# Kernel optimization log

Measured on AMD Instinct MI355X. Metric: run time of the kernel, lower is better.

Reference implementation:

```python
import jax, jax.numpy as jnp
import numpy as np

B, N, D_IN, H, L, HEADS = 8, 1024, 64, 128, 2, 4
HEAD_DIM = H // HEADS
EPS = 1e-5


def setup_inputs() -> dict:
    key = jax.random.key(0)
    ks = jax.random.split(key, 20)
    x = jax.random.normal(ks[0], (B, N, D_IN), dtype=jnp.float32)
    adj = jax.random.randint(ks[1], (B, N, N), 0, 2).astype(jnp.float32)
    s = lambda fan_in: 1.0 / np.sqrt(fan_in)
    enc_w = jax.random.uniform(ks[2], (H, D_IN), minval=-s(D_IN), maxval=s(D_IN))
    enc_b = jax.random.uniform(ks[3], (H,), minval=-s(D_IN), maxval=s(D_IN))
    # per-layer stacked projection weights, torch Linear layout [out,in]
    def mk(k, shape):
        return jax.random.uniform(k, shape, minval=-s(H), maxval=s(H))
    q_w = mk(ks[4], (L, H, H)); q_b = mk(ks[5], (L, H))
    k_w = mk(ks[6], (L, H, H)); k_b = mk(ks[7], (L, H))
    v_w = mk(ks[8], (L, H, H)); v_b = mk(ks[9], (L, H))
    o_w = mk(ks[10], (L, H, H)); o_b = mk(ks[11], (L, H))
    ln_g = jnp.ones((L, H), jnp.float32)
    ln_b = jnp.zeros((L, H), jnp.float32)
    out_w = mk(ks[12], (H, H)); out_b = mk(ks[13], (H,))
    return {"x": x, "adj": adj, "enc_w": enc_w, "enc_b": enc_b,
            "q_w": q_w, "q_b": q_b, "k_w": k_w, "k_b": k_b,
            "v_w": v_w, "v_b": v_b, "o_w": o_w, "o_b": o_b,
            "ln_g": ln_g, "ln_b": ln_b, "out_w": out_w, "out_b": out_b}


def _layernorm(x, g, b):
    mu = jnp.mean(x, axis=-1, keepdims=True)
    var = jnp.var(x, axis=-1, keepdims=True)
    return (x - mu) * jax.lax.rsqrt(var + EPS) * g + b


def _gat_layer(h, adj, qw, qb, kw, kb, vw, vb, ow, ob):
    b, n, _ = h.shape
    q = (h @ qw.T + qb).reshape(b, n, HEADS, HEAD_DIM)
    k = (h @ kw.T + kb).reshape(b, n, HEADS, HEAD_DIM)
    v = (h @ vw.T + vb).reshape(b, n, HEADS, HEAD_DIM)
    scale = HEAD_DIM ** -0.5
    attn = jnp.einsum('bihd,bjhd->bhij', q, k) * scale
    mask = adj[:, None, :, :]  # (b,1,n,n)
    attn = jnp.where(mask == 0, -jnp.inf, attn)
    a = jax.nn.softmax(attn, axis=-1)
    a = jnp.nan_to_num(a, nan=0.0)  # rows with no neighbours -> 0
    out = jnp.einsum('bhij,bjhd->bihd', a, v).reshape(b, n, H)
    return out @ ow.T + ob


def reference(x, adj, enc_w, enc_b, q_w, q_b, k_w, k_b, v_w, v_b,
              o_w, o_b, ln_g, ln_b, out_w, out_b):
    h = jax.nn.relu(x @ enc_w.T + enc_b)
    for i in range(L):
        h_new = _gat_layer(h, adj, q_w[i], q_b[i], k_w[i], k_b[i],
                           v_w[i], v_b[i], o_w[i], o_b[i])
        h = jax.nn.relu(_layernorm(h_new, ln_g[i], ln_b[i])) + h
    return h @ out_w.T + out_b
```

## Files before the change

kernel.cpp:

```cpp
#include <hip/hip_runtime.h>

#define B 8
#define N 1024
#define D_IN 64
#define H 128
#define HEADS 4
#define HD 32
#define L 2
#define EPS 1e-5f
#define NEG_BIG -1e30f
#define SCALE 0.17677669529663687f

typedef __attribute__((ext_vector_type(8))) short bf16x8;
typedef __attribute__((ext_vector_type(4))) float f32x4;

__device__ __forceinline__ unsigned short f2bf(float f) {
    unsigned u = __float_as_uint(f);
    u = u + 0x7fffu + ((u >> 16) & 1u);
    return (unsigned short)(u >> 16);
}
__device__ __forceinline__ float bf2f(unsigned short s) {
    return __uint_as_float(((unsigned)s) << 16);
}
__device__ __forceinline__ void gload_lds16(const void* g, void* l) {
    __builtin_amdgcn_global_load_lds(
        (const __attribute__((address_space(1))) unsigned int*)g,
        (__attribute__((address_space(3))) unsigned int*)l,
        16, 0, 0);
}

__global__ __launch_bounds__(256) void pack_kernel(
    const float* __restrict__ adj, unsigned* __restrict__ mb) {
    int wd = blockIdx.x * 256 + threadIdx.x;
    const float4* src = (const float4*)(adj + (size_t)wd * 32);
    unsigned m = 0;
    #pragma unroll
    for (int c = 0; c < 8; ++c) {
        float4 f = src[c];
        if (f.x != 0.0f) m |= 1u << (c * 4 + 0);
        if (f.y != 0.0f) m |= 1u << (c * 4 + 1);
        if (f.z != 0.0f) m |= 1u << (c * 4 + 2);
        if (f.w != 0.0f) m |= 1u << (c * 4 + 3);
    }
    mb[wd] = m;
}

__global__ __launch_bounds__(256) void prep_kernel(
    const float* __restrict__ x, const float* __restrict__ enc_w,
    const float* __restrict__ q_w, const float* __restrict__ k_w,
    const float* __restrict__ v_w, const float* __restrict__ q_b,
    const float* __restrict__ k_b, const float* __restrict__ v_b,
    const float* __restrict__ o_w, const float* __restrict__ out_w,
    unsigned short* __restrict__ x_bf, unsigned short* __restrict__ wenc,
    unsigned short* __restrict__ wqkv, float* __restrict__ bqkv,
    unsigned short* __restrict__ woh, unsigned short* __restrict__ wol,
    unsigned short* __restrict__ wfh, unsigned short* __restrict__ wfl) {
    int id = blockIdx.x * 256 + threadIdx.x;
    const int XN = B * N * D_IN;
    const int WE = H * D_IN;
    const int WQ = L * 3 * H * H;
    const int BQ = L * 3 * H;
    const int WO = L * H * H;
    const int WF = H * H;
    if (id < XN) { x_bf[id] = f2bf(x[id]); return; }
    id -= XN;
    if (id < WE) { wenc[id] = f2bf(enc_w[id]); return; }
    id -= WE;
    if (id < WQ) {
        int layer = id / (3 * H * H);
        int r = id % (3 * H * H);
        int mat = r / (H * H);
        int e = r % (H * H);
        const float* src = mat == 0 ? q_w : (mat == 1 ? k_w : v_w);
        float f = src[layer * H * H + e];
        if (mat == 0) f *= SCALE;
        wqkv[id] = f2bf(f);
        return;
    }
    id -= WQ;
    if (id < BQ) {
        int layer = id / (3 * H);
        int r = id % (3 * H);
        int mat = r / H;
        int e = r % H;
        const float* src = mat == 0 ? q_b : (mat == 1 ? k_b : v_b);
        float f = src[layer * H + e];
        if (mat == 0) f *= SCALE;
        bqkv[id] = f;
        return;
    }
    id -= BQ;
    if (id < WO) {
        float f = o_w[id];
        unsigned short hi = f2bf(f);
        woh[id] = hi;
        wol[id] = f2bf(f - bf2f(hi));
        return;
    }
    id -= WO;
    if (id < WF) {
        float f = out_w[id];
        unsigned short hi = f2bf(f);
        wfh[id] = hi;
        wfl[id] = f2bf(f - bf2f(hi));
    }
}

__global__ __launch_bounds__(256) void enc_kernel(
    const unsigned short* __restrict__ x_bf, const unsigned short* __restrict__ wenc,
    const float* __restrict__ eb, float* __restrict__ h, unsigned short* __restrict__ h_bf) {
    __shared__ unsigned short wt[H * D_IN];
    __shared__ unsigned short at[64 * D_IN];
    const int t = threadIdx.x;
    const int r0 = blockIdx.x * 64;
    const int w = t >> 6, lane = t & 63, g = lane >> 4, c16 = lane & 15;

    #pragma unroll
    for (int i = 0; i < 4; ++i) {
        int ci = i * 256 + t, row = ci >> 3, cr = ci & 7;
        gload_lds16(wenc + row * 64 + (cr ^ (row & 7)) * 8, (char*)wt + (i * 4 + w) * 1024);
    }
    #pragma unroll
    for (int i = 0; i < 2; ++i) {
        int ci = i * 256 + t, row = ci >> 3, cr = ci & 7;
        gload_lds16(x_bf + (size_t)(r0 + row) * 64 + (cr ^ (row & 7)) * 8,
                    (char*)at + (i * 4 + w) * 1024);
    }
    __syncthreads();

    const int arow = w * 16 + c16;
    bf16x8 a0 = *(const bf16x8*)(at + arow * 64 + ((g ^ (arow & 7)) * 8));
    bf16x8 a1 = *(const bf16x8*)(at + arow * 64 + (((4 + g) ^ (arow & 7)) * 8));
    f32x4 acc[8];
    #pragma unroll
    for (int sub = 0; sub < 8; ++sub) {
        int bcol = sub * 16 + c16;
        bf16x8 b0 = *(const bf16x8*)(wt + bcol * 64 + ((g ^ (bcol & 7)) * 8));
        bf16x8 b1 = *(const bf16x8*)(wt + bcol * 64 + (((4 + g) ^ (bcol & 7)) * 8));
        f32x4 z = {0.f, 0.f, 0.f, 0.f};
        z = __builtin_amdgcn_mfma_f32_16x16x32_bf16(a0, b0, z, 0, 0, 0);
        acc[sub] = __builtin_amdgcn_mfma_f32_16x16x32_bf16(a1, b1, z, 0, 0, 0);
    }
    #pragma unroll
    for (int sub = 0; sub < 8; ++sub) {
        int col = sub * 16 + c16;
        float bias = eb[col];
        #pragma unroll
        for (int rr = 0; rr < 4; ++rr) {
            int row = r0 + w * 16 + g * 4 + rr;
            float v = fmaxf(acc[sub][rr] + bias, 0.0f);
            h[(size_t)row * H + col] = v;
            h_bf[(size_t)row * H + col] = f2bf(v);
        }
    }
}

__global__ __launch_bounds__(256) void qkv_kernel(
    const unsigned short* __restrict__ h_bf, const unsigned short* __restrict__ wqkv_l,
    const float* __restrict__ bqkv_l,
    unsigned short* __restrict__ q, unsigned short* __restrict__ k,
    unsigned short* __restrict__ vT) {
    __shared__ unsigned short wt[192 * 128];
    __shared__ unsigned short at[64 * 128];
    const int t = threadIdx.x;
    const int r0 = (blockIdx.x >> 1) * 64;
    const int ch = blockIdx.x & 1;
    const int w = t >> 6, lane = t & 63, g = lane >> 4, c16 = lane & 15;
    const unsigned short* wsrc = wqkv_l + (size_t)ch * 192 * 128;

    #pragma unroll
    for (int i = 0; i < 12; ++i) {
        int ci = i * 256 + t, row = ci >> 4, cr = ci & 15;
        gload_lds16(wsrc + (size_t)row * 128 + (cr ^ (row & 7)) * 8,
                    (char*)wt + (i * 4 + w) * 1024);
    }
    #pragma unroll
    for (int i = 0; i < 4; ++i) {
        int ci = i * 256 + t, row = ci >> 4, cr = ci & 15;
        gload_lds16(h_bf + (size_t)(r0 + row) * 128 + (cr ^ (row & 7)) * 8,
                    (char*)at + (i * 4 + w) * 1024);
    }
    __syncthreads();

    const int arow = w * 16 + c16;
    bf16x8 a[4];
    #pragma unroll
    for (int ks = 0; ks < 4; ++ks)
        a[ks] = *(const bf16x8*)(at + arow * 128 + (((ks * 4 + g) ^ (arow & 7)) * 8));

    f32x4 acc[12];
    #pragma unroll
    for (int sub = 0; sub < 12; ++sub) {
        int bcol = sub * 16 + c16;
        f32x4 z = {0.f, 0.f, 0.f, 0.f};
        #pragma unroll
        for (int ks = 0; ks < 4; ++ks) {
            bf16x8 bb = *(const bf16x8*)(wt + (size_t)bcol * 128 + (((ks * 4 + g) ^ (bcol & 7)) * 8));
            z = __builtin_amdgcn_mfma_f32_16x16x32_bf16(a[ks], bb, z, 0, 0, 0);
        }
        acc[sub] = z;
    }
    #pragma unroll
    for (int sub = 0; sub < 12; ++sub) {
        int gcol = ch * 192 + sub * 16 + c16;
        int mat = gcol >> 7;
        int colin = gcol & 127;
        float bias = bqkv_l[mat * H + colin];
        if (mat < 2) {
            unsigned short* dst = mat == 0 ? q : k;
            #pragma unroll
            for (int rr = 0; rr < 4; ++rr) {
                int row = r0 + w * 16 + g * 4 + rr;
                dst[(size_t)row * H + colin] = f2bf(acc[sub][rr] + bias);
            }
        } else {
            int hd = colin >> 5, d = colin & 31;
            int bb = r0 >> 10;
            int jbase = (r0 & (N - 1)) + w * 16 + g * 4;
            int pos = (jbase & ~63) + ((((jbase >> 3) & 7) ^ (d & 7)) << 3) + (jbase & 7);
            float v0 = acc[sub][0] + bias, v1 = acc[sub][1] + bias;
            float v2 = acc[sub][2] + bias, v3 = acc[sub][3] + bias;
            unsigned lo, hi;
            asm("v_cvt_pk_bf16_f32 %0, %1, %2" : "=v"(lo) : "v"(v0), "v"(v1));
            asm("v_cvt_pk_bf16_f32 %0, %1, %2" : "=v"(hi) : "v"(v2), "v"(v3));
            uint2 pk2; pk2.x = lo; pk2.y = hi;
            *(uint2*)(vT + ((size_t)(bb * HEADS + hd) * HD + d) * N + pos) = pk2;
        }
    }
}

__global__ __launch_bounds__(256) void attn_kernel(
    const unsigned short* __restrict__ qg, const unsigned short* __restrict__ kg,
    const unsigned short* __restrict__ vTg, const unsigned* __restrict__ mb,
    float* __restrict__ ao) {
    __shared__ unsigned short qt[64 * 32];
    __shared__ unsigned short kt[2][128 * 32];
    __shared__ unsigned short vt[2][32 * 128];
    __shared__ unsigned short pl[4][16 * 136];

    const int bid = blockIdx.x;
    const int itile = bid & 15;
    const int head = (bid >> 4) & 3;
    const int b = bid >> 6;
    const int i0 = itile * 64;
    const int bh = b * HEADS + head;

    const int t = threadIdx.x;
    const int w = t >> 6;
    const int lane = t & 63;
    const int g = lane >> 4;
    const int c16 = lane & 15;

    const int srow = t >> 2;
    const int sch = (t & 3) ^ ((t >> 2) & 3);

    gload_lds16(qg + ((size_t)(b * N + i0 + srow)) * H + head * HD + sch * 8,
                (char*)qt + w * 1024);
    #pragma unroll
    for (int i = 0; i < 2; ++i)
        gload_lds16(kg + ((size_t)(b * N + i * 64 + srow)) * H + head * HD + sch * 8,
                    (char*)kt[0] + i * 4096 + w * 1024);
    #pragma unroll
    for (int i = 0; i < 2; ++i) {
        int d = i * 16 + (t >> 4), c = t & 15;
        gload_lds16(vTg + ((size_t)bh * HD + d) * N + c * 8,
                    (char*)vt[0] + i * 4096 + w * 1024);
    }
    const unsigned* mrow = mb + (size_t)(b * N + i0 + w * 16 + c16) * (N / 32);
    uint4 am = *(const uint4*)mrow;

    __syncthreads();

    const int swq = c16 & 3;
    const bf16x8 qfrag = *(const bf16x8*)(qt + (w * 16 + c16) * 32 + ((g ^ swq) * 8));

    f32x4 oacc[2];
    oacc[0] = (f32x4){0.f, 0.f, 0.f, 0.f};
    oacc[1] = (f32x4){0.f, 0.f, 0.f, 0.f};
    float mrun = NEG_BIG, lrun = 0.0f;

    for (int jt = 0; jt < 8; ++jt) {
        const int cur = jt & 1;
        uint4 amn;
        if (jt < 7) {
            const int j0n = (jt + 1) * 128;
            #pragma unroll
            for (int i = 0; i < 2; ++i)
                gload_lds16(kg + ((size_t)(b * N + j0n + i * 64 + srow)) * H + head * HD + sch * 8,
                            (char*)kt[cur ^ 1] + i * 4096 + w * 1024);
            #pragma unroll
            for (int i = 0; i < 2; ++i) {
                int d = i * 16 + (t >> 4), c = t & 15;
                gload_lds16(vTg + ((size_t)bh * HD + d) * N + j0n + c * 8,
                            (char*)vt[cur ^ 1] + i * 4096 + w * 1024);
            }
            amn = *(const uint4*)(mrow + (jt + 1) * 4);
        }
        f32x4 sacc[8];
        #pragma unroll
        for (int jsub = 0; jsub < 8; ++jsub) {
            bf16x8 kfrag = *(const bf16x8*)(kt[cur] + (jsub * 16 + c16) * 32 + ((g ^ swq) * 8));
            f32x4 z = {0.f, 0.f, 0.f, 0.f};
            sacc[jsub] = __builtin_amdgcn_mfma_f32_16x16x32_bf16(kfrag, qfrag, z, 0, 0, 0);
        }
        float mx = NEG_BIG;
        #pragma unroll
        for (int jsub = 0; jsub < 8; ++jsub) {
            int wsel = jsub >> 1;
            unsigned mw = wsel == 0 ? am.x : wsel == 1 ? am.y : wsel == 2 ? am.z : am.w;
            #pragma unroll
            for (int r = 0; r < 4; ++r) {
                bool alive = (mw >> ((jsub & 1) * 16 + g * 4 + r)) & 1u;
                float s = alive ? sacc[jsub][r] : NEG_BIG;
                sacc[jsub][r] = s;
                mx = fmaxf(mx, s);
            }
        }
        mx = fmaxf(mx, __shfl_xor(mx, 16));
        mx = fmaxf(mx, __shfl_xor(mx, 32));
        float mnew = fmaxf(mrun, mx);
        float sf = __expf(mrun - mnew);
        mrun = mnew;
        float rs = 0.0f;
        #pragma unroll
        for (int jsub = 0; jsub < 8; ++jsub)
            #pragma unroll
            for (int r = 0; r < 4; ++r) {
                float pv = (sacc[jsub][r] > -0.9e30f) ? __expf(sacc[jsub][r] - mnew) : 0.0f;
                sacc[jsub][r] = pv;
                rs += pv;
            }
        rs += __shfl_xor(rs, 16);
        rs += __shfl_xor(rs, 32);
        lrun = lrun * sf + rs;
        #pragma unroll
        for (int jsub = 0; jsub < 8; ++jsub) {
            unsigned lo, hi;
            asm("v_cvt_pk_bf16_f32 %0, %1, %2" : "=v"(lo) : "v"(sacc[jsub][0]), "v"(sacc[jsub][1]));
            asm("v_cvt_pk_bf16_f32 %0, %1, %2" : "=v"(hi) : "v"(sacc[jsub][2]), "v"(sacc[jsub][3]));
            uint2 pk2; pk2.x = lo; pk2.y = hi;
            *(uint2*)(&pl[w][c16 * 136 + jsub * 16 + g * 4]) = pk2;
        }
        #pragma unroll
        for (int dsub = 0; dsub < 2; ++dsub)
            #pragma unroll
            for (int r = 0; r < 4; ++r)
                oacc[dsub][r] *= sf;
        asm volatile("s_waitcnt lgkmcnt(0)" ::: "memory");
        #pragma unroll
        for (int ks = 0; ks < 4; ++ks) {
            bf16x8 pa = *(const bf16x8*)(&pl[w][c16 * 136 + ks * 32 + g * 8]);
            #pragma unroll
            for (int dsub = 0; dsub < 2; ++dsub) {
                int cj = ks * 4 + g;
                bf16x8 va = *(const bf16x8*)(vt[cur] + (dsub * 16 + c16) * 128 +
                                             (cj >> 3) * 64 + (((cj & 7) ^ (c16 & 7)) * 8));
                oacc[dsub] = __builtin_amdgcn_mfma_f32_16x16x32_bf16(va, pa, oacc[dsub], 0, 0, 0);
            }
        }
        if (jt < 7) {
            am = amn;
            __syncthreads();
        }
    }
    float inv = (lrun > 0.0f) ? (1.0f / lrun) : 0.0f;
    #pragma unroll
    for (int dsub = 0; dsub < 2; ++dsub) {
        float4 o;
        o.x = oacc[dsub][0] * inv; o.y = oacc[dsub][1] * inv;
        o.z = oacc[dsub][2] * inv; o.w = oacc[dsub][3] * inv;
        *(float4*)(ao + ((size_t)(b * N + i0 + w * 16 + c16)) * H +
                   head * HD + dsub * 16 + g * 4) = o;
    }
}

__device__ __forceinline__ void stage_split(
    const float* __restrict__ src, unsigned short* hi, unsigned short* lo, int t) {
    #pragma unroll
    for (int it = 0; it < 8; ++it) {
        int idx4 = it * 256 + t;
        int row = idx4 >> 5, c4 = (idx4 & 31) * 4;
        float4 f = ((const float4*)src)[idx4];
        unsigned short h0 = f2bf(f.x), h1 = f2bf(f.y), h2 = f2bf(f.z), h3 = f2bf(f.w);
        unsigned short l0 = f2bf(f.x - bf2f(h0)), l1 = f2bf(f.y - bf2f(h1));
        unsigned short l2 = f2bf(f.z - bf2f(h2)), l3 = f2bf(f.w - bf2f(h3));
        *(unsigned*)(hi + row * 130 + c4)     = (unsigned)h0 | ((unsigned)h1 << 16);
        *(unsigned*)(hi + row * 130 + c4 + 2) = (unsigned)h2 | ((unsigned)h3 << 16);
        *(unsigned*)(lo + row * 130 + c4)     = (unsigned)l0 | ((unsigned)l1 << 16);
        *(unsigned*)(lo + row * 130 + c4 + 2) = (unsigned)l2 | ((unsigned)l3 << 16);
    }
}

__device__ __forceinline__ void split_gemm(
    const unsigned short* ah, const unsigned short* al,
    const unsigned short* wh, const unsigned short* wl,
    int arow, int g, int c16, f32x4* acc) {
    bf16x8 ahf[4], alf[4];
    #pragma unroll
    for (int ks = 0; ks < 4; ++ks) {
        ahf[ks] = *(const bf16x8*)(ah + arow * 130 + ks * 32 + g * 8);
        alf[ks] = *(const bf16x8*)(al + arow * 130 + ks * 32 + g * 8);
    }
    #pragma unroll
    for (int sub = 0; sub < 8; ++sub) {
        int bcol = sub * 16 + c16;
        f32x4 z = {0.f, 0.f, 0.f, 0.f};
        #pragma unroll
        for (int ks = 0; ks < 4; ++ks) {
            bf16x8 bh = *(const bf16x8*)(wh + bcol * 128 + (((ks * 4 + g) ^ (bcol & 7)) * 8));
            bf16x8 bl = *(const bf16x8*)(wl + bcol * 128 + (((ks * 4 + g) ^ (bcol & 7)) * 8));
            z = __builtin_amdgcn_mfma_f32_16x16x32_bf16(ahf[ks], bh, z, 0, 0, 0);
            z = __builtin_amdgcn_mfma_f32_16x16x32_bf16(alf[ks], bh, z, 0, 0, 0);
            z = __builtin_amdgcn_mfma_f32_16x16x32_bf16(ahf[ks], bl, z, 0, 0, 0);
        }
        acc[sub] = z;
    }
}

__device__ __forceinline__ void stage_w(const unsigned short* __restrict__ src,
                                        unsigned short* dst, int t, int w) {
    #pragma unroll
    for (int i = 0; i < 8; ++i) {
        int ci = i * 256 + t, row = ci >> 4, cr = ci & 15;
        gload_lds16(src + (size_t)row * 128 + (cr ^ (row & 7)) * 8,
                    (char*)dst + (i * 4 + w) * 1024);
    }
}

__global__ __launch_bounds__(256) void oln_kernel(
    const float* __restrict__ ao, const unsigned short* __restrict__ woh_l,
    const unsigned short* __restrict__ wol_l, const float* __restrict__ ob,
    const float* __restrict__ lng, const float* __restrict__ lnb,
    float* __restrict__ h, unsigned short* __restrict__ h_bf) {
    __shared__ unsigned short ah[64 * 130], al[64 * 130];
    __shared__ unsigned short wh[128 * 128], wl[128 * 128];
    const int t = threadIdx.x;
    const int r0 = blockIdx.x * 64;
    const int w = t >> 6, lane = t & 63, g = lane >> 4, c16 = lane & 15;

    stage_w(woh_l, wh, t, w);
    stage_w(wol_l, wl, t, w);
    stage_split(ao + (size_t)r0 * H, ah, al, t);
    __syncthreads();

    const int arow = w * 16 + c16;
    f32x4 acc[8];
    split_gemm(ah, al, wh, wl, arow, g, c16, acc);

    float val[8][4], s1[4] = {0, 0, 0, 0}, s2[4] = {0, 0, 0, 0};
    #pragma unroll
    for (int sub = 0; sub < 8; ++sub) {
        int col = sub * 16 + c16;
        float bias = ob[col];
        #pragma unroll
        for (int rr = 0; rr < 4; ++rr) {
            float vv = acc[sub][rr] + bias;
            val[sub][rr] = vv;
            s1[rr] += vv;
            s2[rr] += vv * vv;
        }
    }
    #pragma unroll
    for (int rr = 0; rr < 4; ++rr) {
        #pragma unroll
        for (int off = 1; off < 16; off <<= 1) {
            s1[rr] += __shfl_xor(s1[rr], off);
            s2[rr] += __shfl_xor(s2[rr], off);
        }
    }
    #pragma unroll
    for (int rr = 0; rr < 4; ++rr) {
        float mu = s1[rr] * (1.0f / H);
        float var = s2[rr] * (1.0f / H) - mu * mu;
        float rsn = rsqrtf(var + EPS);
        int row = r0 + w * 16 + g * 4 + rr;
        #pragma unroll
        for (int sub = 0; sub < 8; ++sub) {
            int col = sub * 16 + c16;
            float y = (val[sub][rr] - mu) * rsn * lng[col] + lnb[col];
            float hn = fmaxf(y, 0.0f) + h[(size_t)row * H + col];
            h[(size_t)row * H + col] = hn;
            h_bf[(size_t)row * H + col] = f2bf(hn);
        }
    }
}

__global__ __launch_bounds__(256) void olnfinal_kernel(
    const float* __restrict__ ao, const unsigned short* __restrict__ woh_l,
    const unsigned short* __restrict__ wol_l, const float* __restrict__ ob,
    const float* __restrict__ lng, const float* __restrict__ lnb,
    const float* __restrict__ h, const unsigned short* __restrict__ wfh,
    const unsigned short* __restrict__ wfl, const float* __restrict__ fb,
    float* __restrict__ out) {
    __shared__ unsigned short ah[64 * 130], al[64 * 130];
    __shared__ unsigned short wh[128 * 128], wl[128 * 128];
    const int t = threadIdx.x;
    const int r0 = blockIdx.x * 64;
    const int w = t >> 6, lane = t & 63, g = lane >> 4, c16 = lane & 15;

    stage_w(woh_l, wh, t, w);
    stage_w(wol_l, wl, t, w);
    stage_split(ao + (size_t)r0 * H, ah, al, t);
    __syncthreads();

    const int arow = w * 16 + c16;
    f32x4 acc[8];
    split_gemm(ah, al, wh, wl, arow, g, c16, acc);

    float val[8][4], s1[4] = {0, 0, 0, 0}, s2[4] = {0, 0, 0, 0};
    #pragma unroll
    for (int sub = 0; sub < 8; ++sub) {
        int col = sub * 16 + c16;
        float bias = ob[col];
        #pragma unroll
        for (int rr = 0; rr < 4; ++rr) {
            float vv = acc[sub][rr] + bias;
            val[sub][rr] = vv;
            s1[rr] += vv;
            s2[rr] += vv * vv;
        }
    }
    #pragma unroll
    for (int rr = 0; rr < 4; ++rr) {
        #pragma unroll
        for (int off = 1; off < 16; off <<= 1) {
            s1[rr] += __shfl_xor(s1[rr], off);
            s2[rr] += __shfl_xor(s2[rr], off);
        }
    }
    __syncthreads();
    #pragma unroll
    for (int rr = 0; rr < 4; ++rr) {
        float mu = s1[rr] * (1.0f / H);
        float var = s2[rr] * (1.0f / H) - mu * mu;
        float rsn = rsqrtf(var + EPS);
        int row = w * 16 + g * 4 + rr;
        #pragma unroll
        for (int sub = 0; sub < 8; ++sub) {
            int col = sub * 16 + c16;
            float y = (val[sub][rr] - mu) * rsn * lng[col] + lnb[col];
            float hn = fmaxf(y, 0.0f) + h[(size_t)(r0 + row) * H + col];
            unsigned short hi = f2bf(hn);
            ah[row * 130 + col] = hi;
            al[row * 130 + col] = f2bf(hn - bf2f(hi));
        }
    }
    stage_w(wfh, wh, t, w);
    stage_w(wfl, wl, t, w);
    __syncthreads();

    f32x4 fac[8];
    split_gemm(ah, al, wh, wl, arow, g, c16, fac);
    #pragma unroll
    for (int sub = 0; sub < 8; ++sub) {
        int col = sub * 16 + c16;
        float bias = fb[col];
        #pragma unroll
        for (int rr = 0; rr < 4; ++rr) {
            int row = r0 + w * 16 + g * 4 + rr;
            out[(size_t)row * H + col] = fac[sub][rr] + bias;
        }
    }
}

extern "C" void kernel_launch(void* const* d_in, const int* in_sizes, int n_in,
                              void* d_out, int out_size, void* d_ws, size_t ws_size,
                              hipStream_t stream) {
    const float* x     = (const float*)d_in[0];
    const float* adj   = (const float*)d_in[1];
    const float* enc_w = (const float*)d_in[2];
    const float* enc_b = (const float*)d_in[3];
    const float* q_w   = (const float*)d_in[4];
    const float* q_b   = (const float*)d_in[5];
    const float* k_w   = (const float*)d_in[6];
    const float* k_b   = (const float*)d_in[7];
    const float* v_w   = (const float*)d_in[8];
    const float* v_b   = (const float*)d_in[9];
    const float* o_w   = (const float*)d_in[10];
    const float* o_b   = (const float*)d_in[11];
    const float* ln_g  = (const float*)d_in[12];
    const float* ln_b  = (const float*)d_in[13];
    const float* out_w = (const float*)d_in[14];
    const float* out_b = (const float*)d_in[15];

    const size_t BNH = (size_t)B * N * H;
    float* h  = (float*)d_ws;
    float* ao = h + BNH;
    unsigned short* h_bf = (unsigned short*)(ao + BNH);
    unsigned short* qb = h_bf + BNH;
    unsigned short* kb = qb + BNH;
    unsigned short* vT = kb + BNH;
    unsigned* mbits = (unsigned*)(vT + BNH);
    unsigned short* x_bf = (unsigned short*)(mbits + (size_t)B * N * N / 32);
    unsigned short* wenc = x_bf + (size_t)B * N * D_IN;
    unsigned short* wqkv = wenc + H * D_IN;
    float* bqkv = (float*)(wqkv + (size_t)L * 3 * H * H);
    unsigned short* woh = (unsigned short*)(bqkv + L * 3 * H);
    unsigned short* wol = woh + (size_t)L * H * H;
    unsigned short* wfh = wol + (size_t)L * H * H;
    unsigned short* wfl = wfh + (size_t)H * H;

    pack_kernel<<<B * N * N / 32 / 256, 256, 0, stream>>>(adj, mbits);
    const int prep_total = B * N * D_IN + H * D_IN + L * 3 * H * H + L * 3 * H
                         + L * H * H + H * H;
    prep_kernel<<<(prep_total + 255) / 256, 256, 0, stream>>>(
        x, enc_w, q_w, k_w, v_w, q_b, k_b, v_b, o_w, out_w,
        x_bf, wenc, wqkv, bqkv, woh, wol, wfh, wfl);
    enc_kernel<<<B * N / 64, 256, 0, stream>>>(x_bf, wenc, enc_b, h, h_bf);

    qkv_kernel<<<B * N / 32, 256, 0, stream>>>(h_bf, wqkv, bqkv, qb, kb, vT);
    attn_kernel<<<B * HEADS * (N / 64), 256, 0, stream>>>(qb, kb, vT, mbits, ao);
    oln_kernel<<<B * N / 64, 256, 0, stream>>>(
        ao, woh, wol, o_b, ln_g, ln_b, h, h_bf);
    qkv_kernel<<<B * N / 32, 256, 0, stream>>>(
        h_bf, wqkv + (size_t)3 * H * H, bqkv + 3 * H, qb, kb, vT);
    attn_kernel<<<B * HEADS * (N / 64), 256, 0, stream>>>(qb, kb, vT, mbits, ao);
    olnfinal_kernel<<<B * N / 64, 256, 0, stream>>>(
        ao, woh + (size_t)H * H, wol + (size_t)H * H, o_b + H,
        ln_g + H, ln_b + H, h, wfh, wfl, out_b, (float*)d_out);
}
```

Before: 95.21 us.

## Halve row tiles in enc/oln kernels, use exp2 softmax, add MFMA priority hints

```diff
diff --git a/kernel.cpp b/kernel.cpp
--- a/kernel.cpp
+++ b/kernel.cpp
@@ -9,7 +9,7 @@
 #define L 2
 #define EPS 1e-5f
 #define NEG_BIG -1e30f
-#define SCALE 0.17677669529663687f
+#define QSCALE (0.17677669529663687f * 1.4426950408889634f)
 
 typedef __attribute__((ext_vector_type(8))) short bf16x8;
 typedef __attribute__((ext_vector_type(4))) float f32x4;
@@ -73,7 +73,7 @@
         int e = r % (H * H);
         const float* src = mat == 0 ? q_w : (mat == 1 ? k_w : v_w);
         float f = src[layer * H * H + e];
-        if (mat == 0) f *= SCALE;
+        if (mat == 0) f *= QSCALE;
         wqkv[id] = f2bf(f);
         return;
     }
@@ -85,7 +85,7 @@
         int e = r % H;
         const float* src = mat == 0 ? q_b : (mat == 1 ? k_b : v_b);
         float f = src[layer * H + e];
-        if (mat == 0) f *= SCALE;
+        if (mat == 0) f *= QSCALE;
         bqkv[id] = f;
         return;
     }
@@ -110,31 +110,31 @@
     const unsigned short* __restrict__ x_bf, const unsigned short* __restrict__ wenc,
     const float* __restrict__ eb, float* __restrict__ h, unsigned short* __restrict__ h_bf) {
     __shared__ unsigned short wt[H * D_IN];
-    __shared__ unsigned short at[64 * D_IN];
+    __shared__ unsigned short at[32 * D_IN];
     const int t = threadIdx.x;
-    const int r0 = blockIdx.x * 64;
+    const int r0 = blockIdx.x * 32;
     const int w = t >> 6, lane = t & 63, g = lane >> 4, c16 = lane & 15;
+    const int rw = w & 1, chw = w >> 1;
 
     #pragma unroll
     for (int i = 0; i < 4; ++i) {
         int ci = i * 256 + t, row = ci >> 3, cr = ci & 7;
         gload_lds16(wenc + row * 64 + (cr ^ (row & 7)) * 8, (char*)wt + (i * 4 + w) * 1024);
     }
-    #pragma unroll
-    for (int i = 0; i < 2; ++i) {
-        int ci = i * 256 + t, row = ci >> 3, cr = ci & 7;
+    {
+        int row = t >> 3, cr = t & 7;
         gload_lds16(x_bf + (size_t)(r0 + row) * 64 + (cr ^ (row & 7)) * 8,
-                    (char*)at + (i * 4 + w) * 1024);
-    }
-    __syncthreads();
-
-    const int arow = w * 16 + c16;
+                    (char*)at + w * 1024);
+    }
+    __syncthreads();
+
+    const int arow = rw * 16 + c16;
     bf16x8 a0 = *(const bf16x8*)(at + arow * 64 + ((g ^ (arow & 7)) * 8));
     bf16x8 a1 = *(const bf16x8*)(at + arow * 64 + (((4 + g) ^ (arow & 7)) * 8));
-    f32x4 acc[8];
-    #pragma unroll
-    for (int sub = 0; sub < 8; ++sub) {
-        int bcol = sub * 16 + c16;
+    f32x4 acc[4];
+    #pragma unroll
+    for (int sub = 0; sub < 4; ++sub) {
+        int bcol = chw * 64 + sub * 16 + c16;
         bf16x8 b0 = *(const bf16x8*)(wt + bcol * 64 + ((g ^ (bcol & 7)) * 8));
         bf16x8 b1 = *(const bf16x8*)(wt + bcol * 64 + (((4 + g) ^ (bcol & 7)) * 8));
         f32x4 z = {0.f, 0.f, 0.f, 0.f};
@@ -142,12 +142,12 @@
         acc[sub] = __builtin_amdgcn_mfma_f32_16x16x32_bf16(a1, b1, z, 0, 0, 0);
     }
     #pragma unroll
-    for (int sub = 0; sub < 8; ++sub) {
-        int col = sub * 16 + c16;
+    for (int sub = 0; sub < 4; ++sub) {
+        int col = chw * 64 + sub * 16 + c16;
         float bias = eb[col];
         #pragma unroll
         for (int rr = 0; rr < 4; ++rr) {
-            int row = r0 + w * 16 + g * 4 + rr;
+            int row = r0 + rw * 16 + g * 4 + rr;
             float v = fmaxf(acc[sub][rr] + bias, 0.0f);
             h[(size_t)row * H + col] = v;
             h_bf[(size_t)row * H + col] = f2bf(v);
@@ -297,12 +297,14 @@
             amn = *(const uint4*)(mrow + (jt + 1) * 4);
         }
         f32x4 sacc[8];
+        __builtin_amdgcn_s_setprio(1);
         #pragma unroll
         for (int jsub = 0; jsub < 8; ++jsub) {
             bf16x8 kfrag = *(const bf16x8*)(kt[cur] + (jsub * 16 + c16) * 32 + ((g ^ swq) * 8));
             f32x4 z = {0.f, 0.f, 0.f, 0.f};
             sacc[jsub] = __builtin_amdgcn_mfma_f32_16x16x32_bf16(kfrag, qfrag, z, 0, 0, 0);
         }
+        __builtin_amdgcn_s_setprio(0);
         float mx = NEG_BIG;
         #pragma unroll
         for (int jsub = 0; jsub < 8; ++jsub) {
@@ -319,14 +321,14 @@
         mx = fmaxf(mx, __shfl_xor(mx, 16));
         mx = fmaxf(mx, __shfl_xor(mx, 32));
         float mnew = fmaxf(mrun, mx);
-        float sf = __expf(mrun - mnew);
+        float sf = exp2f(mrun - mnew);
         mrun = mnew;
         float rs = 0.0f;
         #pragma unroll
         for (int jsub = 0; jsub < 8; ++jsub)
             #pragma unroll
             for (int r = 0; r < 4; ++r) {
-                float pv = (sacc[jsub][r] > -0.9e30f) ? __expf(sacc[jsub][r] - mnew) : 0.0f;
+                float pv = exp2f(sacc[jsub][r] - mnew);
                 sacc[jsub][r] = pv;
                 rs += pv;
             }
@@ -347,6 +349,7 @@
             for (int r = 0; r < 4; ++r)
                 oacc[dsub][r] *= sf;
         asm volatile("s_waitcnt lgkmcnt(0)" ::: "memory");
+        __builtin_amdgcn_s_setprio(1);
         #pragma unroll
         for (int ks = 0; ks < 4; ++ks) {
             bf16x8 pa = *(const bf16x8*)(&pl[w][c16 * 136 + ks * 32 + g * 8]);
@@ -358,6 +361,7 @@
                 oacc[dsub] = __builtin_amdgcn_mfma_f32_16x16x32_bf16(va, pa, oacc[dsub], 0, 0, 0);
             }
         }
+        __builtin_amdgcn_s_setprio(0);
         if (jt < 7) {
             am = amn;
             __syncthreads();
@@ -374,10 +378,10 @@
     }
 }
 
-__device__ __forceinline__ void stage_split(
+__device__ __forceinline__ void stage_split32(
     const float* __restrict__ src, unsigned short* hi, unsigned short* lo, int t) {
     #pragma unroll
-    for (int it = 0; it < 8; ++it) {
+    for (int it = 0; it < 4; ++it) {
         int idx4 = it * 256 + t;
         int row = idx4 >> 5, c4 = (idx4 & 31) * 4;
         float4 f = ((const float4*)src)[idx4];
@@ -391,10 +395,10 @@
     }
 }
 
-__device__ __forceinline__ void split_gemm(
+__device__ __forceinline__ void split_gemm4(
     const unsigned short* ah, const unsigned short* al,
     const unsigned short* wh, const unsigned short* wl,
-    int arow, int g, int c16, f32x4* acc) {
+    int arow, int g, int c16, int bcol0, f32x4* acc) {
     bf16x8 ahf[4], alf[4];
     #pragma unroll
     for (int ks = 0; ks < 4; ++ks) {
@@ -402,8 +406,8 @@
         alf[ks] = *(const bf16x8*)(al + arow * 130 + ks * 32 + g * 8);
     }
     #pragma unroll
-    for (int sub = 0; sub < 8; ++sub) {
-        int bcol = sub * 16 + c16;
+    for (int sub = 0; sub < 4; ++sub) {
+        int bcol = bcol0 + sub * 16 + c16;
         f32x4 z = {0.f, 0.f, 0.f, 0.f};
         #pragma unroll
         for (int ks = 0; ks < 4; ++ks) {
@@ -432,25 +436,27 @@
     const unsigned short* __restrict__ wol_l, const float* __restrict__ ob,
     const float* __restrict__ lng, const float* __restrict__ lnb,
     float* __restrict__ h, unsigned short* __restrict__ h_bf) {
-    __shared__ unsigned short ah[64 * 130], al[64 * 130];
+    __shared__ unsigned short ah[32 * 130], al[32 * 130];
     __shared__ unsigned short wh[128 * 128], wl[128 * 128];
+    __shared__ float red1[2][32], red2[2][32];
     const int t = threadIdx.x;
-    const int r0 = blockIdx.x * 64;
+    const int r0 = blockIdx.x * 32;
     const int w = t >> 6, lane = t & 63, g = lane >> 4, c16 = lane & 15;
+    const int rw = w & 1, chw = w >> 1;
 
     stage_w(woh_l, wh, t, w);
     stage_w(wol_l, wl, t, w);
-    stage_split(ao + (size_t)r0 * H, ah, al, t);
-    __syncthreads();
-
-    const int arow = w * 16 + c16;
-    f32x4 acc[8];
-    split_gemm(ah, al, wh, wl, arow, g, c16, acc);
-
-    float val[8][4], s1[4] = {0, 0, 0, 0}, s2[4] = {0, 0, 0, 0};
-    #pragma unroll
-    for (int sub = 0; sub < 8; ++sub) {
-        int col = sub * 16 + c16;
+    stage_split32(ao + (size_t)r0 * H, ah, al, t);
+    __syncthreads();
+
+    const int arow = rw * 16 + c16;
+    f32x4 acc[4];
+    split_gemm4(ah, al, wh, wl, arow, g, c16, chw * 64, acc);
+
+    float val[4][4], s1[4] = {0, 0, 0, 0}, s2[4] = {0, 0, 0, 0};
+    #pragma unroll
+    for (int sub = 0; sub < 4; ++sub) {
+        int col = chw * 64 + sub * 16 + c16;
         float bias = ob[col];
         #pragma unroll
         for (int rr = 0; rr < 4; ++rr) {
@@ -468,15 +474,26 @@
             s2[rr] += __shfl_xor(s2[rr], off);
         }
     }
+    if (c16 == 0) {
+        #pragma unroll
+        for (int rr = 0; rr < 4; ++rr) {
+            red1[chw][rw * 16 + g * 4 + rr] = s1[rr];
+            red2[chw][rw * 16 + g * 4 + rr] = s2[rr];
+        }
+    }
+    __syncthreads();
     #pragma unroll
     for (int rr = 0; rr < 4; ++rr) {
-        float mu = s1[rr] * (1.0f / H);
-        float var = s2[rr] * (1.0f / H) - mu * mu;
+        int rl = rw * 16 + g * 4 + rr;
+        float t1 = red1[0][rl] + red1[1][rl];
+        float t2 = red2[0][rl] + red2[1][rl];
+        float mu = t1 * (1.0f / H);
+        float var = t2 * (1.0f / H) - mu * mu;
         float rsn = rsqrtf(var + EPS);
-        int row = r0 + w * 16 + g * 4 + rr;
-        #pragma unroll
-        for (int sub = 0; sub < 8; ++sub) {
-            int col = sub * 16 + c16;
+        int row = r0 + rl;
+        #pragma unroll
+        for (int sub = 0; sub < 4; ++sub) {
+            int col = chw * 64 + sub * 16 + c16;
             float y = (val[sub][rr] - mu) * rsn * lng[col] + lnb[col];
             float hn = fmaxf(y, 0.0f) + h[(size_t)row * H + col];
             h[(size_t)row * H + col] = hn;
@@ -492,25 +509,27 @@
     const float* __restrict__ h, const unsigned short* __restrict__ wfh,
     const unsigned short* __restrict__ wfl, const float* __restrict__ fb,
     float* __restrict__ out) {
-    __shared__ unsigned short ah[64 * 130], al[64 * 130];
+    __shared__ unsigned short ah[32 * 130], al[32 * 130];
     __shared__ unsigned short wh[128 * 128], wl[128 * 128];
+    __shared__ float red1[2][32], red2[2][32];
     const int t = threadIdx.x;
-    const int r0 = blockIdx.x * 64;
+    const int r0 = blockIdx.x * 32;
     const int w = t >> 6, lane = t & 63, g = lane >> 4, c16 = lane & 15;
+    const int rw = w & 1, chw = w >> 1;
 
     stage_w(woh_l, wh, t, w);
     stage_w(wol_l, wl, t, w);
-    stage_split(ao + (size_t)r0 * H, ah, al, t);
-    __syncthreads();
-
-    const int arow = w * 16 + c16;
-    f32x4 acc[8];
-    split_gemm(ah, al, wh, wl, arow, g, c16, acc);
-
-    float val[8][4], s1[4] = {0, 0, 0, 0}, s2[4] = {0, 0, 0, 0};
-    #pragma unroll
-    for (int sub = 0; sub < 8; ++sub) {
-        int col = sub * 16 + c16;
+    stage_split32(ao + (size_t)r0 * H, ah, al, t);
+    __syncthreads();
+
+    const int arow = rw * 16 + c16;
+    f32x4 acc[4];
+    split_gemm4(ah, al, wh, wl, arow, g, c16, chw * 64, acc);
+
+    float val[4][4], s1[4] = {0, 0, 0, 0}, s2[4] = {0, 0, 0, 0};
+    #pragma unroll
+    for (int sub = 0; sub < 4; ++sub) {
+        int col = chw * 64 + sub * 16 + c16;
         float bias = ob[col];
         #pragma unroll
         for (int rr = 0; rr < 4; ++rr) {
@@ -528,36 +547,45 @@
             s2[rr] += __shfl_xor(s2[rr], off);
         }
     }
+    if (c16 == 0) {
+        #pragma unroll
+        for (int rr = 0; rr < 4; ++rr) {
+            red1[chw][rw * 16 + g * 4 + rr] = s1[rr];
+            red2[chw][rw * 16 + g * 4 + rr] = s2[rr];
+        }
+    }
     __syncthreads();
     #pragma unroll
     for (int rr = 0; rr < 4; ++rr) {
-        float mu = s1[rr] * (1.0f / H);
-        float var = s2[rr] * (1.0f / H) - mu * mu;
+        int rl = rw * 16 + g * 4 + rr;
+        float t1 = red1[0][rl] + red1[1][rl];
+        float t2 = red2[0][rl] + red2[1][rl];
+        float mu = t1 * (1.0f / H);
+        float var = t2 * (1.0f / H) - mu * mu;
         float rsn = rsqrtf(var + EPS);
-        int row = w * 16 + g * 4 + rr;
-        #pragma unroll
-        for (int sub = 0; sub < 8; ++sub) {
-            int col = sub * 16 + c16;
+        #pragma unroll
+        for (int sub = 0; sub < 4; ++sub) {
+            int col = chw * 64 + sub * 16 + c16;
             float y = (val[sub][rr] - mu) * rsn * lng[col] + lnb[col];
-            float hn = fmaxf(y, 0.0f) + h[(size_t)(r0 + row) * H + col];
+            float hn = fmaxf(y, 0.0f) + h[(size_t)(r0 + rl) * H + col];
             unsigned short hi = f2bf(hn);
-            ah[row * 130 + col] = hi;
-            al[row * 130 + col] = f2bf(hn - bf2f(hi));
+            ah[rl * 130 + col] = hi;
+            al[rl * 130 + col] = f2bf(hn - bf2f(hi));
         }
     }
     stage_w(wfh, wh, t, w);
     stage_w(wfl, wl, t, w);
     __syncthreads();
 
-    f32x4 fac[8];
-    split_gemm(ah, al, wh, wl, arow, g, c16, fac);
-    #pragma unroll
-    for (int sub = 0; sub < 8; ++sub) {
-        int col = sub * 16 + c16;
+    f32x4 fac[4];
+    split_gemm4(ah, al, wh, wl, arow, g, c16, chw * 64, fac);
+    #pragma unroll
+    for (int sub = 0; sub < 4; ++sub) {
+        int col = chw * 64 + sub * 16 + c16;
         float bias = fb[col];
         #pragma unroll
         for (int rr = 0; rr < 4; ++rr) {
-            int row = r0 + w * 16 + g * 4 + rr;
+            int row = r0 + rw * 16 + g * 4 + rr;
             out[(size_t)row * H + col] = fac[sub][rr] + bias;
         }
     }
@@ -606,16 +634,16 @@
     prep_kernel<<<(prep_total + 255) / 256, 256, 0, stream>>>(
         x, enc_w, q_w, k_w, v_w, q_b, k_b, v_b, o_w, out_w,
         x_bf, wenc, wqkv, bqkv, woh, wol, wfh, wfl);
-    enc_kernel<<<B * N / 64, 256, 0, stream>>>(x_bf, wenc, enc_b, h, h_bf);
+    enc_kernel<<<B * N / 32, 256, 0, stream>>>(x_bf, wenc, enc_b, h, h_bf);
 
     qkv_kernel<<<B * N / 32, 256, 0, stream>>>(h_bf, wqkv, bqkv, qb, kb, vT);
     attn_kernel<<<B * HEADS * (N / 64), 256, 0, stream>>>(qb, kb, vT, mbits, ao);
-    oln_kernel<<<B * N / 64, 256, 0, stream>>>(
+    oln_kernel<<<B * N / 32, 256, 0, stream>>>(
         ao, woh, wol, o_b, ln_g, ln_b, h, h_bf);
     qkv_kernel<<<B * N / 32, 256, 0, stream>>>(
         h_bf, wqkv + (size_t)3 * H * H, bqkv + 3 * H, qb, kb, vT);
     attn_kernel<<<B * HEADS * (N / 64), 256, 0, stream>>>(qb, kb, vT, mbits, ao);
-    olnfinal_kernel<<<B * N / 64, 256, 0, stream>>>(
+    olnfinal_kernel<<<B * N / 32, 256, 0, stream>>>(
         ao, woh + (size_t)H * H, wol + (size_t)H * H, o_b + H,
         ln_g + H, ln_b + H, h, wfh, wfl, out_b, (float*)d_out);
 }
```

Measured after the change: 95.43 us. Within noise of the previous version (+0.2%).
